# Optimization experiments

Measured on AMD Instinct MI355X. Metric: run time of the kernel, lower is better.

## Reference

```python
import jax, jax.numpy as jnp
import numpy as np

N_HEAD = 8


def setup_inputs() -> dict:
    key = jax.random.key(0)
    k1, k2, k3 = jax.random.split(key, 3)
    B, D, L = 4, 1024, 2048  # channels-first: (batch, feature, seq)
    q = jax.random.normal(k1, (B, D, L), dtype=jnp.float32)
    k = jax.random.normal(k2, (B, D, L), dtype=jnp.float32)
    v = jax.random.normal(k3, (B, D, L), dtype=jnp.float32)
    gamma = jnp.ones((), dtype=jnp.float32)  # nn.Parameter scalar, init 1.0
    return {"q": q, "k": k, "v": v, "gamma": gamma}


def reference(q, k, v, gamma):
    # q, k, v: (B, D, L) channels-first. Head split on feature dim (-2).
    B, Dq, Lq = q.shape
    Dv, Lk = v.shape[-2], v.shape[-1]
    h = N_HEAD
    dq = Dq // h  # per-head query/key dim
    dv = Dv // h  # per-head value dim
    qh = q.reshape(B, h, dq, Lq)
    kh = k.reshape(B, h, dq, Lk)
    vh = v.reshape(B, h, dv, Lk)
    # scale = sqrt(q.size(-2)) AFTER head split, i.e. sqrt(d_head)
    scale = 1.0 / jnp.sqrt(jnp.asarray(dq, dtype=q.dtype))
    # qk: (B, h, Lq, Lk)
    qk = jnp.einsum('bhdq,bhdl->bhql', qh, kh) * scale
    sm = jax.nn.softmax(qk, axis=-1)
    # torch: (sm.unsqueeze(-3) * v.unsqueeze(-2)).sum(-1) == contraction over Lk
    ret = jnp.einsum('bhql,bhdl->bhdq', sm, vh)  # (B, h, dv, Lq)
    ret = ret.reshape(B, Dv, Lq)  # torch: ret.view(-1, v_shape[-2], q_shape[-1])
    return gamma * ret
```

## Files before the change

kernel.cpp:

```cpp
#include <hip/hip_runtime.h>

#define SEQ 2048
#define DHEAD 128
#define BK 32
#define NBH 32

typedef __attribute__((ext_vector_type(8))) short bf16x8;
typedef __attribute__((ext_vector_type(4))) short bf16x4;
typedef __attribute__((ext_vector_type(16))) float f32x16;
typedef __attribute__((ext_vector_type(4))) unsigned int u32x4;

__device__ __forceinline__ unsigned short f2bf(float f) {
    unsigned u = __builtin_bit_cast(unsigned, f);
    u += 0x7fffu + ((u >> 16) & 1u);
    return (unsigned short)(u >> 16);
}

__device__ __forceinline__ float fexp2(float x) {
    float r;
    asm("v_exp_f32 %0, %1" : "=v"(r) : "v"(x));
    return r;
}

__global__ __launch_bounds__(256)
void cvt_kernel(const float* __restrict__ kin, const float* __restrict__ vin,
                unsigned short* __restrict__ kout, unsigned short* __restrict__ vout) {
    const int tid = threadIdx.x;
    if (blockIdx.x < 1024) {
        __shared__ unsigned short tileT[DHEAD][66];
        const int bh = blockIdx.x & 31;
        const int l0 = (blockIdx.x >> 5) * 64;
        const float* ip = kin + (size_t)bh * DHEAD * SEQ;
        const int l4 = (tid & 15) * 4;
        const int dq = tid >> 4;
        for (int pass = 0; pass < 8; ++pass) {
            int d = pass * 16 + dq;
            float4 f = *(const float4*)&ip[(size_t)d * SEQ + l0 + l4];
            unsigned lo = (unsigned)f2bf(f.x) | ((unsigned)f2bf(f.y) << 16);
            unsigned hi = (unsigned)f2bf(f.z) | ((unsigned)f2bf(f.w) << 16);
            *(unsigned*)&tileT[d][l4]     = lo;
            *(unsigned*)&tileT[d][l4 + 2] = hi;
        }
        __syncthreads();
        for (int m = 0; m < 4; ++m) {
            int chunk = m * 256 + tid;
            int c5  = chunk & 31;
            int hi  = (chunk >> 5) & 1;
            int s   = (chunk >> 6) & 7;
            int ktl = chunk >> 9;
            unsigned short tmp[8];
#pragma unroll
            for (int j = 0; j < 8; ++j) tmp[j] = tileT[s * 16 + hi * 8 + j][ktl * 32 + c5];
            size_t gkt = (size_t)(l0 >> 5) + ktl;
            size_t off = ((size_t)bh * 64 + gkt) * 4096 + (size_t)(((s * 2 + hi) * 32 + c5) * 8);
            *(bf16x8*)&kout[off] = *(bf16x8*)tmp;
        }
    } else {
        size_t f = ((size_t)(blockIdx.x - 1024) * 256 + tid) * 8;
        int bh  = (int)(f >> 18);
        int rem = (int)(f & 262143);
        int kt  = rem >> 12;
        int r2  = rem & 4095;
        int dv  = r2 >> 5;
        int e0  = r2 & 31;
        const float* src = vin + ((size_t)bh * DHEAD + dv) * SEQ + kt * BK + e0;
        float4 a = *(const float4*)src;
        float4 b = *(const float4*)(src + 4);
        unsigned short p0[4] = {f2bf(a.x), f2bf(a.y), f2bf(a.z), f2bf(a.w)};
        unsigned short p1[4] = {f2bf(b.x), f2bf(b.y), f2bf(b.z), f2bf(b.w)};
        const int aa = e0 >> 4;
        const int bb = (e0 >> 3) & 1;
        const int u  = dv >> 5;
        const int cv = dv & 31;
        size_t tb = ((size_t)bh * 64 + kt) * 4096;
        size_t o0 = tb + (size_t)((((u * 2 + aa) * 2 + 0) * 32 + cv) * 8 + 4 * bb);
        size_t o1 = tb + (size_t)((((u * 2 + aa) * 2 + 1) * 32 + cv) * 8 + 4 * bb);
        *(bf16x4*)&vout[o0] = *(bf16x4*)p0;
        *(bf16x4*)&vout[o1] = *(bf16x4*)p1;
    }
}

__global__ __launch_bounds__(256, 2)
void attn_main(const float* __restrict__ q,
               const unsigned short* __restrict__ kF,
               const unsigned short* __restrict__ vF,
               const float* __restrict__ gamma,
               float* __restrict__ out) {
    const int tid  = threadIdx.x;
    const int wv   = tid >> 6;
    const int lane = tid & 63;
    const int c5   = lane & 31;
    const int hi   = lane >> 5;
    const int qh   = wv & 1;
    const int dh   = wv >> 1;

    const int bh  = blockIdx.x & 31;
    const int qlb = blockIdx.x >> 5;
    const size_t base = (size_t)bh * SEQ * DHEAD;

    const float* qp = q + base;
    const unsigned short* kb = kF + base;
    const unsigned short* vb = vF + base;
    float* op = out + base;

    const int ql0 = qlb * 128 + qh * 64;
    const float SCL = 0.08838834764831845f * 1.44269504088896340f;

    bf16x8 qf0[8], qf1[8];
#pragma unroll
    for (int s = 0; s < 8; ++s) {
        bf16x8 t0, t1;
#pragma unroll
        for (int j = 0; j < 8; ++j) {
            const size_t drow = (size_t)(s * 16 + hi * 8 + j) * SEQ;
            t0[j] = (short)f2bf(qp[drow + ql0 + c5] * SCL);
            t1[j] = (short)f2bf(qp[drow + ql0 + 32 + c5] * SCL);
        }
        qf0[s] = t0;
        qf1[s] = t1;
    }

    f32x16 acc0[2], acc1[2];
#pragma unroll
    for (int t = 0; t < 2; ++t)
#pragma unroll
        for (int i = 0; i < 16; ++i) { acc0[t][i] = 0.f; acc1[t][i] = 0.f; }
    float lp0 = 0.f, lp1 = 0.f;

    const int ko = lane * 8;
    int voff[4];
#pragma unroll
    for (int t2 = 0; t2 < 2; ++t2)
#pragma unroll
        for (int a = 0; a < 2; ++a)
            voff[t2 * 2 + a] = (((dh * 2 + t2) * 2 + a) * 2 + hi) * 256 + c5 * 8;

    for (int kt = 0; kt < SEQ / BK; ++kt) {
        const unsigned short* kT = kb + (size_t)kt * 4096;
        const unsigned short* vT = vb + (size_t)kt * 4096;

        bf16x8 kf[8], vf[4];
#pragma unroll
        for (int s = 0; s < 8; ++s) kf[s] = *(const bf16x8*)&kT[s * 512 + ko];
#pragma unroll
        for (int t = 0; t < 4; ++t) vf[t] = *(const bf16x8*)&vT[voff[t]];

        f32x16 sT0, sT1;
#pragma unroll
        for (int ii = 0; ii < 16; ++ii) { sT0[ii] = 0.f; sT1[ii] = 0.f; }
        __builtin_amdgcn_s_setprio(1);
#pragma unroll
        for (int s = 0; s < 8; ++s) {
            sT0 = __builtin_amdgcn_mfma_f32_32x32x16_bf16(kf[s], qf0[s], sT0, 0, 0, 0);
            sT1 = __builtin_amdgcn_mfma_f32_32x32x16_bf16(kf[s], qf1[s], sT1, 0, 0, 0);
        }
        __builtin_amdgcn_s_setprio(0);

        unsigned pw0[8], pw1[8];
#pragma unroll
        for (int ii = 0; ii < 8; ++ii) {
            float a0 = fexp2(sT0[2 * ii]);
            float b0 = fexp2(sT0[2 * ii + 1]);
            float a1 = fexp2(sT1[2 * ii]);
            float b1 = fexp2(sT1[2 * ii + 1]);
            lp0 += a0 + b0;
            lp1 += a1 + b1;
            unsigned r0, r1;
            asm("v_cvt_pk_bf16_f32 %0, %1, %2" : "=v"(r0) : "v"(a0), "v"(b0));
            asm("v_cvt_pk_bf16_f32 %0, %1, %2" : "=v"(r1) : "v"(a1), "v"(b1));
            pw0[ii] = r0;
            pw1[ii] = r1;
        }
        bf16x8 p0a = __builtin_bit_cast(bf16x8, (u32x4){pw0[0], pw0[1], pw0[2], pw0[3]});
        bf16x8 p0b = __builtin_bit_cast(bf16x8, (u32x4){pw0[4], pw0[5], pw0[6], pw0[7]});
        bf16x8 p1a = __builtin_bit_cast(bf16x8, (u32x4){pw1[0], pw1[1], pw1[2], pw1[3]});
        bf16x8 p1b = __builtin_bit_cast(bf16x8, (u32x4){pw1[4], pw1[5], pw1[6], pw1[7]});

        __builtin_amdgcn_s_setprio(1);
#pragma unroll
        for (int t2 = 0; t2 < 2; ++t2) {
            acc0[t2] = __builtin_amdgcn_mfma_f32_32x32x16_bf16(vf[t2 * 2],     p0a, acc0[t2], 0, 0, 0);
            acc0[t2] = __builtin_amdgcn_mfma_f32_32x32x16_bf16(vf[t2 * 2 + 1], p0b, acc0[t2], 0, 0, 0);
            acc1[t2] = __builtin_amdgcn_mfma_f32_32x32x16_bf16(vf[t2 * 2],     p1a, acc1[t2], 0, 0, 0);
            acc1[t2] = __builtin_amdgcn_mfma_f32_32x32x16_bf16(vf[t2 * 2 + 1], p1b, acc1[t2], 0, 0, 0);
        }
        __builtin_amdgcn_s_setprio(0);
    }

    const float gm = gamma[0];
    const float L0 = lp0 + __shfl_xor(lp0, 32);
    const float L1 = lp1 + __shfl_xor(lp1, 32);
    const float sc0 = gm / L0;
    const float sc1 = gm / L1;
#pragma unroll
    for (int t2 = 0; t2 < 2; ++t2)
#pragma unroll
        for (int r = 0; r < 16; ++r) {
            int dvr = 32 * (dh * 2 + t2) + (r & 3) + 8 * (r >> 2) + 4 * hi;
            op[(size_t)dvr * SEQ + ql0 + c5]      = acc0[t2][r] * sc0;
            op[(size_t)dvr * SEQ + ql0 + 32 + c5] = acc1[t2][r] * sc1;
        }
}

extern "C" void kernel_launch(void* const* d_in, const int* in_sizes, int n_in,
                              void* d_out, int out_size, void* d_ws, size_t ws_size,
                              hipStream_t stream) {
    (void)in_sizes; (void)n_in; (void)out_size; (void)ws_size;
    const float* q = (const float*)d_in[0];
    const float* k = (const float*)d_in[1];
    const float* v = (const float*)d_in[2];
    const float* g = (const float*)d_in[3];
    float* out = (float*)d_out;

    const size_t PER_T = (size_t)NBH * SEQ * DHEAD;
    unsigned short* kws = (unsigned short*)d_ws;
    unsigned short* vws = kws + PER_T;

    cvt_kernel<<<dim3(1024 + 4096), dim3(256), 0, stream>>>(k, v, kws, vws);
    attn_main<<<dim3(512), dim3(256), 0, stream>>>(q, kws, vws, g, out);
}
```

Measured before the change: 223.8 us.

## Double-buffer K/V register tiles in attention loop and simplify K conversion

The attention main loop now keeps two register sets of K/V fragments and loads the next tile while computing the current one, so global load latency can hide behind the MFMA and exp work. The K conversion kernel drops the shared-memory transpose. Each thread now reads 8 strided floats directly and writes one packed bf16x8 chunk, using a hardware pack-convert, with four times as many blocks. The extra register buffers raise VGPR pressure under launch bounds of 2 blocks per SM, and the strided reads in the converter may coalesce less well.

```diff
diff --git a/kernel.cpp b/kernel.cpp
--- a/kernel.cpp
+++ b/kernel.cpp
@@ -26,37 +26,27 @@
 void cvt_kernel(const float* __restrict__ kin, const float* __restrict__ vin,
                 unsigned short* __restrict__ kout, unsigned short* __restrict__ vout) {
     const int tid = threadIdx.x;
-    if (blockIdx.x < 1024) {
-        __shared__ unsigned short tileT[DHEAD][66];
-        const int bh = blockIdx.x & 31;
-        const int l0 = (blockIdx.x >> 5) * 64;
-        const float* ip = kin + (size_t)bh * DHEAD * SEQ;
-        const int l4 = (tid & 15) * 4;
-        const int dq = tid >> 4;
-        for (int pass = 0; pass < 8; ++pass) {
-            int d = pass * 16 + dq;
-            float4 f = *(const float4*)&ip[(size_t)d * SEQ + l0 + l4];
-            unsigned lo = (unsigned)f2bf(f.x) | ((unsigned)f2bf(f.y) << 16);
-            unsigned hi = (unsigned)f2bf(f.z) | ((unsigned)f2bf(f.w) << 16);
-            *(unsigned*)&tileT[d][l4]     = lo;
-            *(unsigned*)&tileT[d][l4 + 2] = hi;
-        }
-        __syncthreads();
-        for (int m = 0; m < 4; ++m) {
-            int chunk = m * 256 + tid;
-            int c5  = chunk & 31;
-            int hi  = (chunk >> 5) & 1;
-            int s   = (chunk >> 6) & 7;
-            int ktl = chunk >> 9;
-            unsigned short tmp[8];
-#pragma unroll
-            for (int j = 0; j < 8; ++j) tmp[j] = tileT[s * 16 + hi * 8 + j][ktl * 32 + c5];
-            size_t gkt = (size_t)(l0 >> 5) + ktl;
-            size_t off = ((size_t)bh * 64 + gkt) * 4096 + (size_t)(((s * 2 + hi) * 32 + c5) * 8);
-            *(bf16x8*)&kout[off] = *(bf16x8*)tmp;
-        }
+    if (blockIdx.x < 4096) {
+        int idx = blockIdx.x * 256 + tid;
+        int c5 = idx & 31;
+        int hi = (idx >> 5) & 1;
+        int s  = (idx >> 6) & 7;
+        int kt = (idx >> 9) & 63;
+        int bh = idx >> 15;
+        const float* ip = kin + ((size_t)bh * DHEAD + (s * 16 + hi * 8)) * SEQ + kt * 32 + c5;
+        unsigned pw[4];
+#pragma unroll
+        for (int jj = 0; jj < 4; ++jj) {
+            float f0 = ip[(size_t)(2 * jj) * SEQ];
+            float f1 = ip[(size_t)(2 * jj + 1) * SEQ];
+            unsigned r;
+            asm("v_cvt_pk_bf16_f32 %0, %1, %2" : "=v"(r) : "v"(f0), "v"(f1));
+            pw[jj] = r;
+        }
+        size_t off = ((size_t)bh * 64 + kt) * 4096 + (size_t)(((s * 2 + hi) * 32 + c5) * 8);
+        *(u32x4*)&kout[off] = (u32x4){pw[0], pw[1], pw[2], pw[3]};
     } else {
-        size_t f = ((size_t)(blockIdx.x - 1024) * 256 + tid) * 8;
+        size_t f = ((size_t)(blockIdx.x - 4096) * 256 + tid) * 8;
         int bh  = (int)(f >> 18);
         int rem = (int)(f & 262143);
         int kt  = rem >> 12;
@@ -135,16 +125,18 @@
         for (int a = 0; a < 2; ++a)
             voff[t2 * 2 + a] = (((dh * 2 + t2) * 2 + a) * 2 + hi) * 256 + c5 * 8;
 
-    for (int kt = 0; kt < SEQ / BK; ++kt) {
+    bf16x8 kfA[8], vfA[4], kfB[8], vfB[4];
+
+    auto load_tile = [&](int kt, bf16x8* kf, bf16x8* vf) {
         const unsigned short* kT = kb + (size_t)kt * 4096;
         const unsigned short* vT = vb + (size_t)kt * 4096;
-
-        bf16x8 kf[8], vf[4];
 #pragma unroll
         for (int s = 0; s < 8; ++s) kf[s] = *(const bf16x8*)&kT[s * 512 + ko];
 #pragma unroll
         for (int t = 0; t < 4; ++t) vf[t] = *(const bf16x8*)&vT[voff[t]];
-
+    };
+
+    auto compute = [&](const bf16x8* kf, const bf16x8* vf) {
         f32x16 sT0, sT1;
 #pragma unroll
         for (int ii = 0; ii < 16; ++ii) { sT0[ii] = 0.f; sT1[ii] = 0.f; }
@@ -185,6 +177,14 @@
             acc1[t2] = __builtin_amdgcn_mfma_f32_32x32x16_bf16(vf[t2 * 2 + 1], p1b, acc1[t2], 0, 0, 0);
         }
         __builtin_amdgcn_s_setprio(0);
+    };
+
+    load_tile(0, kfA, vfA);
+    for (int kt = 0; kt < SEQ / BK; kt += 2) {
+        load_tile(kt + 1, kfB, vfB);
+        compute(kfA, vfA);
+        if (kt + 2 < SEQ / BK) load_tile(kt + 2, kfA, vfA);
+        compute(kfB, vfB);
     }
 
     const float gm = gamma[0];
@@ -216,6 +216,6 @@
     unsigned short* kws = (unsigned short*)d_ws;
     unsigned short* vws = kws + PER_T;
 
-    cvt_kernel<<<dim3(1024 + 4096), dim3(256), 0, stream>>>(k, v, kws, vws);
+    cvt_kernel<<<dim3(4096 + 4096), dim3(256), 0, stream>>>(k, v, kws, vws);
     attn_main<<<dim3(512), dim3(256), 0, stream>>>(q, kws, vws, g, out);
 }
```

New measurement: 248.5 us. 1.11x slower.
